# Optimization experiments

Hardware: AMD Instinct MI355X
Metric: run time of the kernel (lower is better)

The kernel has to match this reference:

```python
import jax, jax.numpy as jnp
import numpy as np

B, S, D = 2, 2048, 1024
E, N, HID = 8, 4, 4096

def setup_inputs() -> dict:
    key = jax.random.key(0)
    ks = jax.random.split(key, 6)
    x = jax.random.normal(ks[0], (B, S, D), dtype=jnp.float32)
    w_router = jax.random.normal(ks[1], (E, D), dtype=jnp.float32) * 0.02
    A_fc = jax.random.normal(ks[2], (E, N, N, N), dtype=jnp.float32) * 0.5
    S_fc = jax.random.normal(ks[3], (E, N, HID // N, D // N), dtype=jnp.float32) * (1.0 / np.sqrt(D))
    A_proj = jax.random.normal(ks[4], (E, N, N, N), dtype=jnp.float32) * 0.5
    S_proj = jax.random.normal(ks[5], (E, N, D // N, HID // N), dtype=jnp.float32) * (1.0 / np.sqrt(HID))
    return {"x": x, "w_router": w_router, "A_fc": A_fc, "S_fc": S_fc, "A_proj": A_proj, "S_proj": S_proj}

def _phm(Xn, A, S):
    # Xn: [T, n, s_in], S: [n, s_out, s_in], A: [n, n, n] -> [T, n, s_out]
    T_ = jnp.einsum('bkl,iol->bkio', Xn, S)
    return jnp.einsum('ijk,bkio->bjo', A, T_)

def reference(x, w_router, A_fc, S_fc, A_proj, S_proj):
    e_num, n = A_fc.shape[0], A_fc.shape[1]
    d = x.shape[-1]
    flat = x.reshape(-1, d)                      # [T, D]
    T = flat.shape[0]
    logits = flat @ w_router.T                   # [T, E]
    probs = jax.nn.softmax(logits, axis=-1)
    expert_idx = jnp.argmax(logits, axis=-1)     # [T]
    tpe = jnp.zeros((e_num,), flat.dtype).at[expert_idx].add(1.0)
    frac = tpe / T
    aux_loss = jnp.sum(frac * probs.mean(axis=0)) * e_num
    Xn = flat.reshape(T, n, d // n)
    out = jnp.zeros_like(flat)
    for e in range(e_num):                        # small fixed expert loop
        h = _phm(Xn, A_fc[e], S_fc[e]).reshape(T, -1)   # [T, HID]
        h = jnp.where(h >= 0, h, 0.5 * h)               # leaky_relu slope 0.5
        Hn = (h * h).reshape(T, n, -1)
        y = _phm(Hn, A_proj[e], S_proj[e]).reshape(T, d)
        out = out + jnp.where((expert_idx == e)[:, None], y, jnp.zeros((), flat.dtype))
    return out.reshape(x.shape), aux_loss
```

## Files before the change

kernel.cpp:

```cpp
#include <hip/hip_runtime.h>
#include <hip/hip_bf16.h>


#define T_TOK 4096
#define DIM   1024
#define NEXP  8
#define HIDD  4096
#define SLOTS 5120

static constexpr size_t OFF_WFC   = 0;
static constexpr size_t OFF_WPROJ = 67108864ull;
static constexpr size_t OFF_XB    = 134217728ull;
static constexpr size_t OFF_H     = 144703488ull;
static constexpr size_t OFF_BSUM  = 186646528ull;
static constexpr size_t OFF_EIDX  = OFF_BSUM + 1024*8*8;
static constexpr size_t OFF_TOK   = OFF_EIDX + (size_t)T_TOK*4;
static constexpr size_t OFF_CNT   = OFF_TOK + (size_t)SLOTS*4;

typedef __attribute__((ext_vector_type(8))) short short8;
typedef __attribute__((ext_vector_type(4))) float f32x4;

static __device__ __forceinline__ ushort f2bf(float f) {
    __hip_bfloat16 h = __float2bfloat16(f);
    return __builtin_bit_cast(ushort, h);
}

static __device__ __forceinline__ float bf2f(ushort u) {
    return __builtin_bit_cast(float, (unsigned)u << 16);
}

static __device__ __forceinline__ ushort4 f4bf(float4 v) {
    ushort4 b;
    b.x = f2bf(v.x); b.y = f2bf(v.y); b.z = f2bf(v.z); b.w = f2bf(v.w);
    return b;
}

static __device__ __forceinline__ void gload_lds16(const ushort* g, ushort* l) {
    __builtin_amdgcn_global_load_lds((const __attribute__((address_space(1))) void*)g,
                                     (__attribute__((address_space(3))) void*)l,
                                     16, 0, 0);
}

__global__ __launch_bounds__(256) void front_k(const float* __restrict__ x,
                                               const float* __restrict__ wr,
                                               double* __restrict__ bsum,
                                               int* __restrict__ eidx,
                                               ushort* __restrict__ xb)
{
    __shared__ double shp[4][8];
    int tid = threadIdx.x;
    int w = tid >> 6, lane = tid & 63;
    int t = blockIdx.x * 4 + w;
    const float4* xr = (const float4*)(x + (size_t)t * DIM);
    float4 xv[4];
#pragma unroll
    for (int q = 0; q < 4; q++) xv[q] = xr[q * 64 + lane];
    ushort4* xo = (ushort4*)(xb + (size_t)t * DIM);
#pragma unroll
    for (int q = 0; q < 4; q++) xo[q * 64 + lane] = f4bf(xv[q]);
    double lg[8];
#pragma unroll
    for (int e = 0; e < 8; e++) {
        const float4* wv = (const float4*)(wr + (size_t)e * DIM);
        double s = 0.0;
#pragma unroll
        for (int q = 0; q < 4; q++) {
            float4 a = xv[q], b = wv[q * 64 + lane];
            s += (double)a.x * b.x + (double)a.y * b.y + (double)a.z * b.z + (double)a.w * b.w;
        }
#pragma unroll
        for (int d = 1; d < 64; d <<= 1) s += __shfl_xor(s, d);
        lg[e] = s;
    }
    double m = lg[0];
#pragma unroll
    for (int e = 1; e < 8; e++) m = lg[e] > m ? lg[e] : m;
    float ex[8], sum = 0.f;
#pragma unroll
    for (int e = 0; e < 8; e++) { ex[e] = __expf((float)(lg[e] - m)); sum += ex[e]; }
    if (lane < 8) shp[w][lane] = (double)(ex[lane] / sum);
    if (lane == 0) {
        int am = 0; double bv = lg[0];
#pragma unroll
        for (int e = 1; e < 8; e++) if (lg[e] > bv) { bv = lg[e]; am = e; }
        eidx[t] = am;
    }
    __syncthreads();
    if (tid < 8)
        bsum[(size_t)blockIdx.x * 8 + tid] =
            shp[0][tid] + shp[1][tid] + shp[2][tid] + shp[3][tid];
}

__global__ __launch_bounds__(256) void plan_k(const double* __restrict__ bsum,
                                              const int* __restrict__ eidx,
                                              int* __restrict__ counts,
                                              int* __restrict__ offsets,
                                              int* __restrict__ tok,
                                              float* __restrict__ auxout,
                                              const float* __restrict__ Afc,
                                              const float* __restrict__ Sfc,
                                              ushort* __restrict__ Wfc)
{
    __shared__ int hist[256][8];
    __shared__ double red[256][8];
    __shared__ int offs[8];
    __shared__ float Ash[64];
    int tid = threadIdx.x;
    if (blockIdx.x > 0) {
        int b2 = blockIdx.x - 1;
        int e = b2 >> 10, o = b2 & 1023;
        if (tid < 64) Ash[tid] = Afc[e * 64 + tid];
        __syncthreads();
        int k = tid >> 6, lq = tid & 63;
        float4 sv[4];
#pragma unroll
        for (int i = 0; i < 4; i++)
            sv[i] = *(const float4*)&Sfc[((size_t)(e * 4 + i) * 1024 + o) * 256 + lq * 4];
        size_t base = (size_t)e * 4194304ull;
#pragma unroll
        for (int j = 0; j < 4; j++) {
            float a0 = Ash[j * 4 + k], a1 = Ash[16 + j * 4 + k];
            float a2 = Ash[32 + j * 4 + k], a3 = Ash[48 + j * 4 + k];
            float4 v;
            v.x = a0 * sv[0].x + a1 * sv[1].x + a2 * sv[2].x + a3 * sv[3].x;
            v.y = a0 * sv[0].y + a1 * sv[1].y + a2 * sv[2].y + a3 * sv[3].y;
            v.z = a0 * sv[0].z + a1 * sv[1].z + a2 * sv[2].z + a3 * sv[3].z;
            v.w = a0 * sv[0].w + a1 * sv[1].w + a2 * sv[2].w + a3 * sv[3].w;
            *(ushort4*)&Wfc[base + (size_t)(j * 1024 + o) * 1024 + k * 256 + lq * 4] = f4bf(v);
        }
        return;
    }
    for (int i = tid; i < SLOTS; i += 256) tok[i] = -1;
    int base = tid * 16;
    int le[16];
    int lc[8] = {0,0,0,0,0,0,0,0};
#pragma unroll
    for (int j = 0; j < 16; j++) { le[j] = eidx[base + j]; lc[le[j]]++; }
#pragma unroll
    for (int e = 0; e < 8; e++) hist[tid][e] = lc[e];
    __syncthreads();
    for (int s = 1; s < 256; s <<= 1) {
        int v[8];
        if (tid >= s) {
#pragma unroll
            for (int e = 0; e < 8; e++) v[e] = hist[tid - s][e];
        }
        __syncthreads();
        if (tid >= s) {
#pragma unroll
            for (int e = 0; e < 8; e++) hist[tid][e] += v[e];
        }
        __syncthreads();
    }
    int myBase[8];
#pragma unroll
    for (int e = 0; e < 8; e++) myBase[e] = hist[tid][e] - lc[e];
    if (tid == 0) {
        int off = 0;
#pragma unroll
        for (int e = 0; e < 8; e++) {
            int c = hist[255][e];
            counts[e] = c;
            offsets[e] = off; offs[e] = off;
            off += (c + 127) & ~127;
        }
    }
    __syncthreads();
    int cur[8];
#pragma unroll
    for (int e = 0; e < 8; e++) cur[e] = myBase[e];
#pragma unroll
    for (int j = 0; j < 16; j++) {
        int e = le[j];
        tok[offs[e] + cur[e]++] = base + j;
    }
    double ps[8] = {0, 0, 0, 0, 0, 0, 0, 0};
    for (int b = tid; b < 1024; b += 256) {
#pragma unroll
        for (int e = 0; e < 8; e++) ps[e] += bsum[(size_t)b * 8 + e];
    }
#pragma unroll
    for (int e = 0; e < 8; e++) red[tid][e] = ps[e];
    __syncthreads();
    for (int s = 128; s > 0; s >>= 1) {
        if (tid < s) {
#pragma unroll
            for (int e = 0; e < 8; e++) red[tid][e] += red[tid + s][e];
        }
        __syncthreads();
    }
    if (tid == 0) {
        double aux = 0.0;
#pragma unroll
        for (int e = 0; e < 8; e++)
            aux += ((double)hist[255][e] / T_TOK) * (red[0][e] / T_TOK);
        auxout[0] = (float)(aux * NEXP);
    }
}

__global__ __launch_bounds__(256, 2) void mid_k(const ushort* __restrict__ xb,
                                                const ushort* __restrict__ Wfc,
                                                ushort* __restrict__ h,
                                                const int* __restrict__ counts,
                                                const int* __restrict__ offsets,
                                                const int* __restrict__ tok,
                                                const float* __restrict__ Apj,
                                                const float* __restrict__ Spj,
                                                ushort* __restrict__ Wpj)
{
    __shared__ __align__(16) ushort As[128 * 64];
    __shared__ __align__(16) ushort Bs[256 * 64];
    __shared__ float Ashf[64];
    int b = blockIdx.x;
    int tid = threadIdx.x;
    if (b >= 640) {
        int b2 = b - 640;
        int e = b2 >> 8, o = b2 & 255;
        if (tid < 64) Ashf[tid] = Apj[e * 64 + tid];
        __syncthreads();
        float4 sv[4];
#pragma unroll
        for (int i = 0; i < 4; i++)
            sv[i] = *(const float4*)&Spj[((size_t)(e * 4 + i) * 256 + o) * 1024 + tid * 4];
        size_t base = (size_t)e * 4194304ull;
#pragma unroll
        for (int j = 0; j < 4; j++)
#pragma unroll
            for (int k = 0; k < 4; k++) {
                float a0 = Ashf[j * 4 + k], a1 = Ashf[16 + j * 4 + k];
                float a2 = Ashf[32 + j * 4 + k], a3 = Ashf[48 + j * 4 + k];
                float4 v;
                v.x = a0 * sv[0].x + a1 * sv[1].x + a2 * sv[2].x + a3 * sv[3].x;
                v.y = a0 * sv[0].y + a1 * sv[1].y + a2 * sv[2].y + a3 * sv[3].y;
                v.z = a0 * sv[0].z + a1 * sv[1].z + a2 * sv[2].z + a3 * sv[3].z;
                v.w = a0 * sv[0].w + a1 * sv[1].w + a2 * sv[2].w + a3 * sv[3].w;
                *(ushort4*)&Wpj[base + (size_t)(j * 256 + o) * 4096 + k * 1024 + tid * 4] = f4bf(v);
            }
        return;
    }
    constexpr int KDIM = 1024;
    constexpr int NDIM = 4096;
    int r = b >> 3;
    int nb = (b & 7) * 2 + r / 40;
    int ms = r % 40;
    int e = -1, mt = 0, acct = 0;
#pragma unroll
    for (int i = 0; i < 8; i++) {
        int tiles = (counts[i] + 127) >> 7;
        if (e < 0 && ms < acct + tiles) { e = i; mt = ms - acct; }
        acct += tiles;
    }
    if (e < 0) return;
    int m_base = offsets[e] + mt * 128;
    int n_base = nb * 256;
    int w = tid >> 6, lane = tid & 63;
    int wm = w >> 1, wn = w & 1;
    const ushort* Bb = Wfc + (size_t)e * NDIM * KDIM + (size_t)n_base * KDIM;
    int lr = lane >> 3;
    int lcs = (((lane & 7) ^ lr) << 3);
    const ushort* arow[4];
#pragma unroll
    for (int i = 0; i < 4; i++) {
        int sl = m_base + i * 32 + w * 8 + lr;
        int rt = tok[sl]; if (rt < 0) rt = 0;
        arow[i] = xb + (size_t)rt * KDIM + lcs;
    }
    f32x4 acc[4][8];
#pragma unroll
    for (int i = 0; i < 4; i++)
#pragma unroll
        for (int j = 0; j < 8; j++) acc[i][j] = (f32x4){0.f, 0.f, 0.f, 0.f};

    for (int t = 0; t < KDIM / 64; t++) {
        int k0 = t * 64;
#pragma unroll
        for (int i = 0; i < 4; i++)
            gload_lds16(arow[i] + k0, &As[(i * 32 + w * 8) * 64]);
#pragma unroll
        for (int i = 0; i < 8; i++) {
            int r0 = i * 32 + w * 8;
            gload_lds16(Bb + (size_t)(r0 + lr) * KDIM + k0 + lcs, &Bs[r0 * 64]);
        }
        __syncthreads();
#pragma unroll
        for (int ks = 0; ks < 2; ks++) {
            short8 a[4], bfr[8];
            int ca = (((ks * 4 + (lane >> 4)) ^ (lane & 7)) << 3);
#pragma unroll
            for (int f = 0; f < 4; f++)
                a[f] = *(const short8*)&As[(wm * 64 + f * 16 + (lane & 15)) * 64 + ca];
#pragma unroll
            for (int f = 0; f < 8; f++)
                bfr[f] = *(const short8*)&Bs[(wn * 128 + f * 16 + (lane & 15)) * 64 + ca];
#pragma unroll
            for (int mf = 0; mf < 4; mf++)
#pragma unroll
                for (int nf = 0; nf < 8; nf++)
                    acc[mf][nf] = __builtin_amdgcn_mfma_f32_16x16x32_bf16(a[mf], bfr[nf], acc[mf][nf], 0, 0, 0);
        }
        __syncthreads();
    }

    int col0 = n_base + wn * 128;
    int row0 = wm * 64 + (lane >> 4) * 4;
#pragma unroll
    for (int mf = 0; mf < 4; mf++)
#pragma unroll
        for (int nf = 0; nf < 8; nf++) {
            int col = col0 + nf * 16 + (lane & 15);
#pragma unroll
            for (int rg = 0; rg < 4; rg++) {
                float v = acc[mf][nf][rg];
                v = v >= 0.f ? v : 0.5f * v;
                v = v * v;
                h[(size_t)(m_base + row0 + mf * 16 + rg) * NDIM + col] = f2bf(v);
            }
        }
}

__global__ __launch_bounds__(256, 2) void proj_k(const ushort* __restrict__ h,
                                                 const ushort* __restrict__ Wpj,
                                                 ushort* __restrict__ Part,
                                                 const int* __restrict__ counts,
                                                 const int* __restrict__ offsets)
{
    __shared__ __align__(16) ushort As[128 * 64];
    __shared__ __align__(16) ushort Bs[256 * 64];
    constexpr int KDIM = 4096;
    constexpr int NDIM = 1024;
    constexpr int KSUB = 2048;
    int b = blockIdx.x;
    int nb = (b & 7) >> 1;
    int split = b & 1;
    int ms = b >> 3;
    int e = -1, mt = 0, acct = 0;
#pragma unroll
    for (int i = 0; i < 8; i++) {
        int tiles = (counts[i] + 127) >> 7;
        if (e < 0 && ms < acct + tiles) { e = i; mt = ms - acct; }
        acct += tiles;
    }
    if (e < 0) return;
    int m_base = offsets[e] + mt * 128;
    int n_base = nb * 256;
    int tid = threadIdx.x, w = tid >> 6, lane = tid & 63;
    int wm = w >> 1, wn = w & 1;
    int lr = lane >> 3;
    int lcs = (((lane & 7) ^ lr) << 3);
    int kbase = split * KSUB;
    const ushort* Bb = Wpj + (size_t)e * NDIM * KDIM + (size_t)n_base * KDIM + kbase;
    const ushort* arow[4];
#pragma unroll
    for (int i = 0; i < 4; i++)
        arow[i] = h + (size_t)(m_base + i * 32 + w * 8 + lr) * KDIM + kbase + lcs;
    f32x4 acc[4][8];
#pragma unroll
    for (int i = 0; i < 4; i++)
#pragma unroll
        for (int j = 0; j < 8; j++) acc[i][j] = (f32x4){0.f, 0.f, 0.f, 0.f};

    for (int t = 0; t < KSUB / 64; t++) {
        int k0 = t * 64;
#pragma unroll
        for (int i = 0; i < 4; i++)
            gload_lds16(arow[i] + k0, &As[(i * 32 + w * 8) * 64]);
#pragma unroll
        for (int i = 0; i < 8; i++) {
            int r0 = i * 32 + w * 8;
            gload_lds16(Bb + (size_t)(r0 + lr) * KDIM + k0 + lcs, &Bs[r0 * 64]);
        }
        __syncthreads();
#pragma unroll
        for (int ks = 0; ks < 2; ks++) {
            short8 a[4], bfr[8];
            int ca = (((ks * 4 + (lane >> 4)) ^ (lane & 7)) << 3);
#pragma unroll
            for (int f = 0; f < 4; f++)
                a[f] = *(const short8*)&As[(wm * 64 + f * 16 + (lane & 15)) * 64 + ca];
#pragma unroll
            for (int f = 0; f < 8; f++)
                bfr[f] = *(const short8*)&Bs[(wn * 128 + f * 16 + (lane & 15)) * 64 + ca];
#pragma unroll
            for (int mf = 0; mf < 4; mf++)
#pragma unroll
                for (int nf = 0; nf < 8; nf++)
                    acc[mf][nf] = __builtin_amdgcn_mfma_f32_16x16x32_bf16(a[mf], bfr[nf], acc[mf][nf], 0, 0, 0);
        }
        __syncthreads();
    }

    ushort* P = Part + (size_t)split * SLOTS * NDIM;
    int col0 = n_base + wn * 128;
    int row0 = wm * 64 + (lane >> 4) * 4;
#pragma unroll
    for (int mf = 0; mf < 4; mf++)
#pragma unroll
        for (int nf = 0; nf < 8; nf++) {
            int col = col0 + nf * 16 + (lane & 15);
#pragma unroll
            for (int rg = 0; rg < 4; rg++)
                P[(size_t)(m_base + row0 + mf * 16 + rg) * NDIM + col] = f2bf(acc[mf][nf][rg]);
        }
}

__global__ __launch_bounds__(256) void reduce_k(const ushort* __restrict__ P,
                                                const int* __restrict__ tok,
                                                float* __restrict__ out)
{
    int slot = blockIdx.x;
    int t = tok[slot];
    if (t < 0) return;
    int i = threadIdx.x;
    const ushort4* p0 = (const ushort4*)(P + (size_t)slot * DIM);
    const ushort4* p1 = (const ushort4*)(P + (size_t)(SLOTS + slot) * DIM);
    ushort4 a = p0[i], b = p1[i];
    float4* o = (float4*)(out + (size_t)t * DIM);
    o[i] = (float4){bf2f(a.x) + bf2f(b.x), bf2f(a.y) + bf2f(b.y),
                    bf2f(a.z) + bf2f(b.z), bf2f(a.w) + bf2f(b.w)};
}

extern "C" void kernel_launch(void* const* d_in, const int* in_sizes, int n_in,
                              void* d_out, int out_size, void* d_ws, size_t ws_size,
                              hipStream_t stream)
{
    const float* x    = (const float*)d_in[0];
    const float* wr   = (const float*)d_in[1];
    const float* A_fc = (const float*)d_in[2];
    const float* S_fc = (const float*)d_in[3];
    const float* A_pj = (const float*)d_in[4];
    const float* S_pj = (const float*)d_in[5];
    float* out = (float*)d_out;
    char* ws = (char*)d_ws;

    ushort* Wfc   = (ushort*)(ws + OFF_WFC);
    ushort* Part  = (ushort*)(ws + OFF_WFC);
    ushort* Wpj   = (ushort*)(ws + OFF_WPROJ);
    ushort* xb    = (ushort*)(ws + OFF_XB);
    ushort* h     = (ushort*)(ws + OFF_H);
    double* bsum  = (double*)(ws + OFF_BSUM);
    int*    eidx  = (int*)(ws + OFF_EIDX);
    int*    tok   = (int*)(ws + OFF_TOK);
    int*    counts  = (int*)(ws + OFF_CNT);
    int*    offsets = counts + 16;

    front_k<<<T_TOK / 4, 256, 0, stream>>>(x, wr, bsum, eidx, xb);
    plan_k<<<1 + 8192, 256, 0, stream>>>(bsum, eidx, counts, offsets, tok,
                                         out + (size_t)T_TOK * DIM,
                                         A_fc, S_fc, Wfc);
    mid_k<<<640 + 2048, 256, 0, stream>>>(xb, Wfc, h, counts, offsets, tok,
                                          A_pj, S_pj, Wpj);
    proj_k<<<320, 256, 0, stream>>>(h, Wpj, Part, counts, offsets);
    reduce_k<<<SLOTS, 256, 0, stream>>>(Part, tok, out);
}
```

Before: 165.1 us.

## Replace expert GEMMs with 256x256 double-buffered 8-wave kernel, split-K 4 for proj

Both expert GEMMs move to one templated kernel that uses 256x256 tiles, 512 threads and double-buffered LDS, with loads interleaved between MFMA phases and setprio around the MFMA blocks. Expert slot padding grows to 256 rows to match the new tile, and the projection GEMM uses 4-way split-K, so the reduce kernel now sums four partials. The projection weight preparation moves from the mid kernel into plan_k so the GEMMs become pure matmul launches. The cost is more padded rows and more partial-sum traffic, plus extra LDS per block, which may limit occupancy.

```diff
diff --git a/kernel.cpp b/kernel.cpp
--- a/kernel.cpp
+++ b/kernel.cpp
@@ -6,16 +6,16 @@
 #define DIM   1024
 #define NEXP  8
 #define HIDD  4096
-#define SLOTS 5120
+#define SLOTS 6144
 
 static constexpr size_t OFF_WFC   = 0;
 static constexpr size_t OFF_WPROJ = 67108864ull;
 static constexpr size_t OFF_XB    = 134217728ull;
-static constexpr size_t OFF_H     = 144703488ull;
-static constexpr size_t OFF_BSUM  = 186646528ull;
-static constexpr size_t OFF_EIDX  = OFF_BSUM + 1024*8*8;
-static constexpr size_t OFF_TOK   = OFF_EIDX + (size_t)T_TOK*4;
-static constexpr size_t OFF_CNT   = OFF_TOK + (size_t)SLOTS*4;
+static constexpr size_t OFF_BSUM  = 142606336ull;
+static constexpr size_t OFF_EIDX  = 142671872ull;
+static constexpr size_t OFF_TOK   = 142688256ull;
+static constexpr size_t OFF_CNT   = 142712832ull;
+static constexpr size_t OFF_H     = 142713856ull;
 
 typedef __attribute__((ext_vector_type(8))) short short8;
 typedef __attribute__((ext_vector_type(4))) float f32x4;
@@ -99,13 +99,41 @@
                                               float* __restrict__ auxout,
                                               const float* __restrict__ Afc,
                                               const float* __restrict__ Sfc,
-                                              ushort* __restrict__ Wfc)
+                                              ushort* __restrict__ Wfc,
+                                              const float* __restrict__ Apj,
+                                              const float* __restrict__ Spj,
+                                              ushort* __restrict__ Wpj)
 {
     __shared__ int hist[256][8];
     __shared__ double red[256][8];
     __shared__ int offs[8];
     __shared__ float Ash[64];
     int tid = threadIdx.x;
+    if (blockIdx.x > 8192) {
+        int b2 = blockIdx.x - 8193;
+        int e = b2 >> 8, o = b2 & 255;
+        if (tid < 64) Ash[tid] = Apj[e * 64 + tid];
+        __syncthreads();
+        float4 sv[4];
+#pragma unroll
+        for (int i = 0; i < 4; i++)
+            sv[i] = *(const float4*)&Spj[((size_t)(e * 4 + i) * 256 + o) * 1024 + tid * 4];
+        size_t base = (size_t)e * 4194304ull;
+#pragma unroll
+        for (int j = 0; j < 4; j++)
+#pragma unroll
+            for (int k = 0; k < 4; k++) {
+                float a0 = Ash[j * 4 + k], a1 = Ash[16 + j * 4 + k];
+                float a2 = Ash[32 + j * 4 + k], a3 = Ash[48 + j * 4 + k];
+                float4 v;
+                v.x = a0 * sv[0].x + a1 * sv[1].x + a2 * sv[2].x + a3 * sv[3].x;
+                v.y = a0 * sv[0].y + a1 * sv[1].y + a2 * sv[2].y + a3 * sv[3].y;
+                v.z = a0 * sv[0].z + a1 * sv[1].z + a2 * sv[2].z + a3 * sv[3].z;
+                v.w = a0 * sv[0].w + a1 * sv[1].w + a2 * sv[2].w + a3 * sv[3].w;
+                *(ushort4*)&Wpj[base + (size_t)(j * 256 + o) * 4096 + k * 1024 + tid * 4] = f4bf(v);
+            }
+        return;
+    }
     if (blockIdx.x > 0) {
         int b2 = blockIdx.x - 1;
         int e = b2 >> 10, o = b2 & 1023;
@@ -162,7 +190,7 @@
             int c = hist[255][e];
             counts[e] = c;
             offsets[e] = off; offs[e] = off;
-            off += (c + 127) & ~127;
+            off += (c + 255) & ~255;
         }
     }
     __syncthreads();
@@ -198,209 +226,171 @@
     }
 }
 
-__global__ __launch_bounds__(256, 2) void mid_k(const ushort* __restrict__ xb,
-                                                const ushort* __restrict__ Wfc,
-                                                ushort* __restrict__ h,
-                                                const int* __restrict__ counts,
-                                                const int* __restrict__ offsets,
-                                                const int* __restrict__ tok,
-                                                const float* __restrict__ Apj,
-                                                const float* __restrict__ Spj,
-                                                ushort* __restrict__ Wpj)
+template <int KDIM, int NDIM, int NSPLIT, bool FC>
+__global__ __launch_bounds__(512, 2) void gemm8_k(const ushort* __restrict__ Abuf,
+                                                  const ushort* __restrict__ Wbuf,
+                                                  ushort* __restrict__ Hout,
+                                                  ushort* __restrict__ Pout,
+                                                  const int* __restrict__ counts,
+                                                  const int* __restrict__ offsets,
+                                                  const int* __restrict__ tok)
 {
-    __shared__ __align__(16) ushort As[128 * 64];
-    __shared__ __align__(16) ushort Bs[256 * 64];
-    __shared__ float Ashf[64];
+    __shared__ __align__(16) ushort As[2][256 * 64];
+    __shared__ __align__(16) ushort Bs[2][256 * 64];
+    constexpr int KSUB = KDIM / NSPLIT;
+    constexpr int NT = KSUB / 64;
     int b = blockIdx.x;
-    int tid = threadIdx.x;
-    if (b >= 640) {
-        int b2 = b - 640;
-        int e = b2 >> 8, o = b2 & 255;
-        if (tid < 64) Ashf[tid] = Apj[e * 64 + tid];
-        __syncthreads();
-        float4 sv[4];
-#pragma unroll
-        for (int i = 0; i < 4; i++)
-            sv[i] = *(const float4*)&Spj[((size_t)(e * 4 + i) * 256 + o) * 1024 + tid * 4];
-        size_t base = (size_t)e * 4194304ull;
-#pragma unroll
-        for (int j = 0; j < 4; j++)
-#pragma unroll
-            for (int k = 0; k < 4; k++) {
-                float a0 = Ashf[j * 4 + k], a1 = Ashf[16 + j * 4 + k];
-                float a2 = Ashf[32 + j * 4 + k], a3 = Ashf[48 + j * 4 + k];
-                float4 v;
-                v.x = a0 * sv[0].x + a1 * sv[1].x + a2 * sv[2].x + a3 * sv[3].x;
-                v.y = a0 * sv[0].y + a1 * sv[1].y + a2 * sv[2].y + a3 * sv[3].y;
-                v.z = a0 * sv[0].z + a1 * sv[1].z + a2 * sv[2].z + a3 * sv[3].z;
-                v.w = a0 * sv[0].w + a1 * sv[1].w + a2 * sv[2].w + a3 * sv[3].w;
-                *(ushort4*)&Wpj[base + (size_t)(j * 256 + o) * 4096 + k * 1024 + tid * 4] = f4bf(v);
-            }
-        return;
-    }
-    constexpr int KDIM = 1024;
-    constexpr int NDIM = 4096;
     int r = b >> 3;
-    int nb = (b & 7) * 2 + r / 40;
-    int ms = r % 40;
+    int nb, split, ms;
+    if (FC) {
+        nb = (b & 7) * 2 + r / 24;
+        split = 0;
+        ms = r % 24;
+    } else {
+        int combo = (b & 7) * 2 + r / 24;
+        nb = combo >> 2;
+        split = combo & 3;
+        ms = r % 24;
+    }
     int e = -1, mt = 0, acct = 0;
 #pragma unroll
     for (int i = 0; i < 8; i++) {
-        int tiles = (counts[i] + 127) >> 7;
+        int tiles = (counts[i] + 255) >> 8;
         if (e < 0 && ms < acct + tiles) { e = i; mt = ms - acct; }
         acct += tiles;
     }
     if (e < 0) return;
-    int m_base = offsets[e] + mt * 128;
-    int n_base = nb * 256;
-    int w = tid >> 6, lane = tid & 63;
-    int wm = w >> 1, wn = w & 1;
-    const ushort* Bb = Wfc + (size_t)e * NDIM * KDIM + (size_t)n_base * KDIM;
-    int lr = lane >> 3;
-    int lcs = (((lane & 7) ^ lr) << 3);
-    const ushort* arow[4];
-#pragma unroll
-    for (int i = 0; i < 4; i++) {
-        int sl = m_base + i * 32 + w * 8 + lr;
-        int rt = tok[sl]; if (rt < 0) rt = 0;
-        arow[i] = xb + (size_t)rt * KDIM + lcs;
-    }
-    f32x4 acc[4][8];
-#pragma unroll
-    for (int i = 0; i < 4; i++)
-#pragma unroll
-        for (int j = 0; j < 8; j++) acc[i][j] = (f32x4){0.f, 0.f, 0.f, 0.f};
-
-    for (int t = 0; t < KDIM / 64; t++) {
-        int k0 = t * 64;
-#pragma unroll
-        for (int i = 0; i < 4; i++)
-            gload_lds16(arow[i] + k0, &As[(i * 32 + w * 8) * 64]);
-#pragma unroll
-        for (int i = 0; i < 8; i++) {
-            int r0 = i * 32 + w * 8;
-            gload_lds16(Bb + (size_t)(r0 + lr) * KDIM + k0 + lcs, &Bs[r0 * 64]);
-        }
-        __syncthreads();
-#pragma unroll
-        for (int ks = 0; ks < 2; ks++) {
-            short8 a[4], bfr[8];
-            int ca = (((ks * 4 + (lane >> 4)) ^ (lane & 7)) << 3);
-#pragma unroll
-            for (int f = 0; f < 4; f++)
-                a[f] = *(const short8*)&As[(wm * 64 + f * 16 + (lane & 15)) * 64 + ca];
-#pragma unroll
-            for (int f = 0; f < 8; f++)
-                bfr[f] = *(const short8*)&Bs[(wn * 128 + f * 16 + (lane & 15)) * 64 + ca];
-#pragma unroll
-            for (int mf = 0; mf < 4; mf++)
-#pragma unroll
-                for (int nf = 0; nf < 8; nf++)
-                    acc[mf][nf] = __builtin_amdgcn_mfma_f32_16x16x32_bf16(a[mf], bfr[nf], acc[mf][nf], 0, 0, 0);
-        }
-        __syncthreads();
-    }
-
-    int col0 = n_base + wn * 128;
-    int row0 = wm * 64 + (lane >> 4) * 4;
-#pragma unroll
-    for (int mf = 0; mf < 4; mf++)
-#pragma unroll
-        for (int nf = 0; nf < 8; nf++) {
-            int col = col0 + nf * 16 + (lane & 15);
-#pragma unroll
-            for (int rg = 0; rg < 4; rg++) {
-                float v = acc[mf][nf][rg];
-                v = v >= 0.f ? v : 0.5f * v;
-                v = v * v;
-                h[(size_t)(m_base + row0 + mf * 16 + rg) * NDIM + col] = f2bf(v);
-            }
-        }
-}
-
-__global__ __launch_bounds__(256, 2) void proj_k(const ushort* __restrict__ h,
-                                                 const ushort* __restrict__ Wpj,
-                                                 ushort* __restrict__ Part,
-                                                 const int* __restrict__ counts,
-                                                 const int* __restrict__ offsets)
-{
-    __shared__ __align__(16) ushort As[128 * 64];
-    __shared__ __align__(16) ushort Bs[256 * 64];
-    constexpr int KDIM = 4096;
-    constexpr int NDIM = 1024;
-    constexpr int KSUB = 2048;
-    int b = blockIdx.x;
-    int nb = (b & 7) >> 1;
-    int split = b & 1;
-    int ms = b >> 3;
-    int e = -1, mt = 0, acct = 0;
-#pragma unroll
-    for (int i = 0; i < 8; i++) {
-        int tiles = (counts[i] + 127) >> 7;
-        if (e < 0 && ms < acct + tiles) { e = i; mt = ms - acct; }
-        acct += tiles;
-    }
-    if (e < 0) return;
-    int m_base = offsets[e] + mt * 128;
+    int m_base = offsets[e] + mt * 256;
     int n_base = nb * 256;
     int tid = threadIdx.x, w = tid >> 6, lane = tid & 63;
-    int wm = w >> 1, wn = w & 1;
+    int wm = w >> 2, wn = w & 3;
     int lr = lane >> 3;
     int lcs = (((lane & 7) ^ lr) << 3);
     int kbase = split * KSUB;
-    const ushort* Bb = Wpj + (size_t)e * NDIM * KDIM + (size_t)n_base * KDIM + kbase;
     const ushort* arow[4];
-#pragma unroll
-    for (int i = 0; i < 4; i++)
-        arow[i] = h + (size_t)(m_base + i * 32 + w * 8 + lr) * KDIM + kbase + lcs;
-    f32x4 acc[4][8];
-#pragma unroll
-    for (int i = 0; i < 4; i++)
-#pragma unroll
-        for (int j = 0; j < 8; j++) acc[i][j] = (f32x4){0.f, 0.f, 0.f, 0.f};
-
-    for (int t = 0; t < KSUB / 64; t++) {
-        int k0 = t * 64;
-#pragma unroll
-        for (int i = 0; i < 4; i++)
-            gload_lds16(arow[i] + k0, &As[(i * 32 + w * 8) * 64]);
-#pragma unroll
-        for (int i = 0; i < 8; i++) {
-            int r0 = i * 32 + w * 8;
-            gload_lds16(Bb + (size_t)(r0 + lr) * KDIM + k0 + lcs, &Bs[r0 * 64]);
-        }
-        __syncthreads();
-#pragma unroll
-        for (int ks = 0; ks < 2; ks++) {
-            short8 a[4], bfr[8];
-            int ca = (((ks * 4 + (lane >> 4)) ^ (lane & 7)) << 3);
-#pragma unroll
-            for (int f = 0; f < 4; f++)
-                a[f] = *(const short8*)&As[(wm * 64 + f * 16 + (lane & 15)) * 64 + ca];
-#pragma unroll
-            for (int f = 0; f < 8; f++)
-                bfr[f] = *(const short8*)&Bs[(wn * 128 + f * 16 + (lane & 15)) * 64 + ca];
-#pragma unroll
-            for (int mf = 0; mf < 4; mf++)
-#pragma unroll
-                for (int nf = 0; nf < 8; nf++)
-                    acc[mf][nf] = __builtin_amdgcn_mfma_f32_16x16x32_bf16(a[mf], bfr[nf], acc[mf][nf], 0, 0, 0);
-        }
-        __syncthreads();
-    }
-
-    ushort* P = Part + (size_t)split * SLOTS * NDIM;
-    int col0 = n_base + wn * 128;
-    int row0 = wm * 64 + (lane >> 4) * 4;
-#pragma unroll
-    for (int mf = 0; mf < 4; mf++)
-#pragma unroll
-        for (int nf = 0; nf < 8; nf++) {
-            int col = col0 + nf * 16 + (lane & 15);
-#pragma unroll
-            for (int rg = 0; rg < 4; rg++)
-                P[(size_t)(m_base + row0 + mf * 16 + rg) * NDIM + col] = f2bf(acc[mf][nf][rg]);
-        }
+    const ushort* brow[4];
+    int adst[4], bdst[4];
+#pragma unroll
+    for (int j = 0; j < 4; j++) {
+        int rrow = (j >> 1) * 128 + (j & 1) * 64 + w * 8;
+        adst[j] = rrow * 64;
+        bdst[j] = rrow * 64;
+        int slot = m_base + rrow + lr;
+        int rt = slot;
+        if (FC) { rt = tok[slot]; if (rt < 0) rt = 0; }
+        arow[j] = Abuf + (size_t)rt * KDIM + kbase + lcs;
+        brow[j] = Wbuf + (size_t)e * NDIM * KDIM + (size_t)(n_base + rrow + lr) * KDIM + kbase + lcs;
+    }
+    f32x4 acc[8][4];
+#pragma unroll
+    for (int i = 0; i < 8; i++)
+#pragma unroll
+        for (int j = 0; j < 4; j++) acc[i][j] = (f32x4){0.f, 0.f, 0.f, 0.f};
+
+    {
+        int k0 = 0;
+#pragma unroll
+        for (int j = 0; j < 4; j++) gload_lds16(arow[j] + k0, &As[0][adst[j]]);
+#pragma unroll
+        for (int j = 0; j < 4; j++) gload_lds16(brow[j] + k0, &Bs[0][bdst[j]]);
+    }
+    asm volatile("s_waitcnt vmcnt(0)" ::: "memory");
+    __builtin_amdgcn_s_barrier();
+
+    int rbA = wm * 128 + (lane & 15);
+    int rbB = wn * 64 + (lane & 15);
+    for (int t = 0; t < NT; t++) {
+        int cur = t & 1, nxt = cur ^ 1;
+        int k1 = (t + 1) * 64;
+        short8 bf[4][2];
+        if (t + 1 < NT) {
+#pragma unroll
+            for (int j = 0; j < 4; j++) gload_lds16(arow[j] + k1, &As[nxt][adst[j]]);
+        }
+#pragma unroll
+        for (int nf = 0; nf < 4; nf++)
+#pragma unroll
+            for (int ks = 0; ks < 2; ks++) {
+                int ca = (((ks * 4 + (lane >> 4)) ^ (lane & 7)) << 3);
+                bf[nf][ks] = *(const short8*)&Bs[cur][(rbB + nf * 16) * 64 + ca];
+            }
+        {
+            short8 af[2][2];
+#pragma unroll
+            for (int mf = 0; mf < 2; mf++)
+#pragma unroll
+                for (int ks = 0; ks < 2; ks++) {
+                    int ca = (((ks * 4 + (lane >> 4)) ^ (lane & 7)) << 3);
+                    af[mf][ks] = *(const short8*)&As[cur][(rbA + mf * 16) * 64 + ca];
+                }
+            __builtin_amdgcn_s_setprio(1);
+#pragma unroll
+            for (int ks = 0; ks < 2; ks++)
+#pragma unroll
+                for (int mf = 0; mf < 2; mf++)
+#pragma unroll
+                    for (int nf = 0; nf < 4; nf++)
+                        acc[mf][nf] = __builtin_amdgcn_mfma_f32_16x16x32_bf16(af[mf][ks], bf[nf][ks], acc[mf][nf], 0, 0, 0);
+            __builtin_amdgcn_s_setprio(0);
+        }
+        __builtin_amdgcn_s_barrier();
+        if (t + 1 < NT) {
+#pragma unroll
+            for (int j = 0; j < 4; j++) gload_lds16(brow[j] + k1, &Bs[nxt][bdst[j]]);
+        }
+#pragma unroll
+        for (int p = 1; p < 4; p++) {
+            short8 af[2][2];
+#pragma unroll
+            for (int mf = 0; mf < 2; mf++)
+#pragma unroll
+                for (int ks = 0; ks < 2; ks++) {
+                    int ca = (((ks * 4 + (lane >> 4)) ^ (lane & 7)) << 3);
+                    af[mf][ks] = *(const short8*)&As[cur][(rbA + (p * 2 + mf) * 16) * 64 + ca];
+                }
+            __builtin_amdgcn_s_setprio(1);
+#pragma unroll
+            for (int ks = 0; ks < 2; ks++)
+#pragma unroll
+                for (int mf = 0; mf < 2; mf++)
+#pragma unroll
+                    for (int nf = 0; nf < 4; nf++)
+                        acc[p * 2 + mf][nf] = __builtin_amdgcn_mfma_f32_16x16x32_bf16(af[mf][ks], bf[nf][ks], acc[p * 2 + mf][nf], 0, 0, 0);
+            __builtin_amdgcn_s_setprio(0);
+            if (p < 3) __builtin_amdgcn_s_barrier();
+        }
+        asm volatile("s_waitcnt vmcnt(0)" ::: "memory");
+        __builtin_amdgcn_s_barrier();
+    }
+
+    int col0 = n_base + wn * 64;
+    int row0 = m_base + wm * 128 + (lane >> 4) * 4;
+    if (FC) {
+#pragma unroll
+        for (int mf = 0; mf < 8; mf++)
+#pragma unroll
+            for (int nf = 0; nf < 4; nf++) {
+                int col = col0 + nf * 16 + (lane & 15);
+#pragma unroll
+                for (int rg = 0; rg < 4; rg++) {
+                    float v = acc[mf][nf][rg];
+                    v = v >= 0.f ? v : 0.5f * v;
+                    v = v * v;
+                    Hout[(size_t)(row0 + mf * 16 + rg) * NDIM + col] = f2bf(v);
+                }
+            }
+    } else {
+        ushort* P = Pout + (size_t)split * SLOTS * NDIM;
+#pragma unroll
+        for (int mf = 0; mf < 8; mf++)
+#pragma unroll
+            for (int nf = 0; nf < 4; nf++) {
+                int col = col0 + nf * 16 + (lane & 15);
+#pragma unroll
+                for (int rg = 0; rg < 4; rg++)
+                    P[(size_t)(row0 + mf * 16 + rg) * NDIM + col] = f2bf(acc[mf][nf][rg]);
+            }
+    }
 }
 
 __global__ __launch_bounds__(256) void reduce_k(const ushort* __restrict__ P,
@@ -411,12 +401,13 @@
     int t = tok[slot];
     if (t < 0) return;
     int i = threadIdx.x;
-    const ushort4* p0 = (const ushort4*)(P + (size_t)slot * DIM);
-    const ushort4* p1 = (const ushort4*)(P + (size_t)(SLOTS + slot) * DIM);
-    ushort4 a = p0[i], b = p1[i];
-    float4* o = (float4*)(out + (size_t)t * DIM);
-    o[i] = (float4){bf2f(a.x) + bf2f(b.x), bf2f(a.y) + bf2f(b.y),
-                    bf2f(a.z) + bf2f(b.z), bf2f(a.w) + bf2f(b.w)};
+    float4 s = (float4){0.f, 0.f, 0.f, 0.f};
+#pragma unroll
+    for (int sp = 0; sp < 4; sp++) {
+        ushort4 a = ((const ushort4*)(P + (size_t)(sp * SLOTS + slot) * DIM))[i];
+        s.x += bf2f(a.x); s.y += bf2f(a.y); s.z += bf2f(a.z); s.w += bf2f(a.w);
+    }
+    ((float4*)(out + (size_t)t * DIM))[i] = s;
 }
 
 extern "C" void kernel_launch(void* const* d_in, const int* in_sizes, int n_in,
@@ -444,11 +435,12 @@
     int*    offsets = counts + 16;
 
     front_k<<<T_TOK / 4, 256, 0, stream>>>(x, wr, bsum, eidx, xb);
-    plan_k<<<1 + 8192, 256, 0, stream>>>(bsum, eidx, counts, offsets, tok,
-                                         out + (size_t)T_TOK * DIM,
-                                         A_fc, S_fc, Wfc);
-    mid_k<<<640 + 2048, 256, 0, stream>>>(xb, Wfc, h, counts, offsets, tok,
-                                          A_pj, S_pj, Wpj);
-    proj_k<<<320, 256, 0, stream>>>(h, Wpj, Part, counts, offsets);
+    plan_k<<<1 + 8192 + 2048, 256, 0, stream>>>(bsum, eidx, counts, offsets, tok,
+                                                out + (size_t)T_TOK * DIM,
+                                                A_fc, S_fc, Wfc, A_pj, S_pj, Wpj);
+    gemm8_k<1024, 4096, 1, true><<<384, 512, 0, stream>>>(xb, Wfc, h, nullptr,
+                                                          counts, offsets, tok);
+    gemm8_k<4096, 1024, 4, false><<<384, 512, 0, stream>>>(h, Wpj, nullptr, Part,
+                                                           counts, offsets, tok);
     reduce_k<<<SLOTS, 256, 0, stream>>>(Part, tok, out);
 }
```

New measurement: 200.8 us. 21.6% more time.
